# Performance work log

Hardware: AMD Instinct MI355X
Metric: run time of the kernel (lower is better)

Reference implementation:

```python
import jax, jax.numpy as jnp
import numpy as np

# DREAMPlace IDXST_IDCT (a.k.a. idsct2): y[u,v] = sum_p sum_q x[p,q] * sin(pi*p*(u+0.5)/M) * cos(pi*q*(v+0.5)/N)
# i.e. IDXST (inverse discrete sine transform, DST-III-like, unnormalized) along the M axis
# and IDCT (DCT-III-like, unnormalized, full weight on k=0) along the N axis.
# Computed with the classic 2N-padded FFT trick using the precomputed twiddles
# expk[k] = exp(-1j*pi*k/(2N)) stored as [N,2] (real, imag), matching precompute_expk.

def _idxt_spectrum(x, expk):
    """F[u] = sum_k x[k] * exp(-1j*pi*k*(2u+1)/(2N)), along last axis.
    Re(F) is the IDCT sum (cos), -Im(F) is the IDXST sum (sin)."""
    N = x.shape[-1]
    c = (x * expk[..., 0]) + 1j * (x * expk[..., 1])  # x[k] * exp(-j*pi*k/(2N))
    z = jnp.concatenate([c, jnp.zeros_like(c)], axis=-1)  # zero-pad to 2N
    return jnp.fft.fft(z, axis=-1)[..., :N]


def idct_1d(x, expk):
    # y[u] = sum_k x[k] cos(pi*k*(2u+1)/(2N))
    return _idxt_spectrum(x, expk).real


def idxst_1d(x, expk):
    # y[u] = sum_k x[k] sin(pi*k*(2u+1)/(2N))
    return -_idxt_spectrum(x, expk).imag


def _make_expk(L):
    k = jnp.arange(L, dtype=jnp.float32) * (np.pi / (2.0 * L))
    return jnp.stack([jnp.cos(k), -jnp.sin(k)], axis=-1)  # exp(-j*pi*k/(2L))


def setup_inputs() -> dict:
    M, N = 4096, 4096
    key = jax.random.key(0)
    x = jax.random.normal(key, (M, N), dtype=jnp.float32)
    return {"x": x, "expkM": _make_expk(M), "expkN": _make_expk(N)}


def reference(x, expkM, expkN):
    # IDCT along the last dim (N), then IDXST along the second-to-last dim (M):
    # idxst(idct(x)^T)^T
    t = idct_1d(x, expkN)                                        # [M, N]
    y = idxst_1d(t.swapaxes(-2, -1), expkM).swapaxes(-2, -1)     # [M, N]
    return y
```

## Files before the change

kernel.cpp:

```cpp
#include <hip/hip_runtime.h>
#include <hip/hip_bf16.h>
#include <stdint.h>
#include <cmath>


typedef __attribute__((ext_vector_type(4))) float f32x4;
typedef __attribute__((ext_vector_type(8))) unsigned short u16x8;
typedef __attribute__((ext_vector_type(8))) __bf16 bf16x8;

__device__ __forceinline__ unsigned short f2bf(float f) {
  union { float f; unsigned u; } v; v.f = f;
  unsigned u = v.u + 0x7fffu + ((v.u >> 16) & 1u);
  return (unsigned short)(u >> 16);
}

__device__ __forceinline__ void gen_half(int idx, u16x8* Pe, u16x8* Po,
                                         int isSin, int jshift, int jmask,
                                         unsigned mask4L, float sc) {
  int i = idx >> jshift;
  int jb = (idx & jmask) * 8;
  unsigned tp = 2u * (unsigned)i + 1u;
  unsigned re = (2u * (unsigned)jb * tp) & mask4L;
  unsigned ro = (re + tp) & mask4L;
  unsigned step = (2u * tp) & mask4L;
  u16x8 pe, po;
#pragma unroll
  for (int t = 0; t < 8; t++) {
    float se_, ce_, so_, co_;
    __sincosf((float)re * sc, &se_, &ce_);
    __sincosf((float)ro * sc, &so_, &co_);
    pe[t] = f2bf(isSin ? se_ : ce_);
    po[t] = f2bf(isSin ? so_ : co_);
    re = (re + step) & mask4L;
    ro = (ro + step) & mask4L;
  }
  Pe[idx] = pe;
  Po[idx] = po;
}

__global__ void prep_kernel(const f32x4* __restrict__ x, u16x8* __restrict__ xe,
                            u16x8* __restrict__ xo, u16x8* __restrict__ Ce,
                            u16x8* __restrict__ Co, u16x8* __restrict__ Se,
                            u16x8* __restrict__ So, int nConvBlocks,
                            int nGenNBlocks, int jshiftN, int jmaskN,
                            unsigned mask4N, float scN, int jshiftM, int jmaskM,
                            unsigned mask4M, float scM) {
  int b = blockIdx.x;
  if (b < nConvBlocks) {
    int idx = b * 256 + threadIdx.x;
    f32x4 a = x[4 * idx], bb = x[4 * idx + 1], c = x[4 * idx + 2],
          d = x[4 * idx + 3];
    u16x8 e, o;
    e[0] = f2bf(a[0]);  o[0] = f2bf(a[1]);  e[1] = f2bf(a[2]);  o[1] = f2bf(a[3]);
    e[2] = f2bf(bb[0]); o[2] = f2bf(bb[1]); e[3] = f2bf(bb[2]); o[3] = f2bf(bb[3]);
    e[4] = f2bf(c[0]);  o[4] = f2bf(c[1]);  e[5] = f2bf(c[2]);  o[5] = f2bf(c[3]);
    e[6] = f2bf(d[0]);  o[6] = f2bf(d[1]);  e[7] = f2bf(d[2]);  o[7] = f2bf(d[3]);
    xe[idx] = e;
    xo[idx] = o;
  } else if (b < nConvBlocks + nGenNBlocks) {
    int idx = (b - nConvBlocks) * 256 + threadIdx.x;
    gen_half(idx, Ce, Co, 0, jshiftN, jmaskN, mask4N, scN);
  } else {
    int idx = (b - nConvBlocks - nGenNBlocks) * 256 + threadIdx.x;
    gen_half(idx, Se, So, 1, jshiftM, jmaskM, mask4M, scM);
  }
}

#define LGKM8()                                             \
  do {                                                      \
    asm volatile("s_waitcnt lgkmcnt(8)" ::: "memory");      \
    __builtin_amdgcn_sched_barrier(0);                      \
  } while (0)
#define LGKM0()                                             \
  do {                                                      \
    asm volatile("s_waitcnt lgkmcnt(0)" ::: "memory");      \
    __builtin_amdgcn_sched_barrier(0);                      \
  } while (0)
#define VMCNT8()                                            \
  do {                                                      \
    asm volatile("s_waitcnt vmcnt(8)" ::: "memory");        \
    __builtin_amdgcn_sched_barrier(0);                      \
  } while (0)
#define VMCNT0()                                            \
  do {                                                      \
    asm volatile("s_waitcnt vmcnt(0)" ::: "memory");        \
    __builtin_amdgcn_sched_barrier(0);                      \
  } while (0)
#define BAR() __builtin_amdgcn_s_barrier()

template <int STAGE>
__global__ __launch_bounds__(256, 2) void fused_gemm_kernel(
    const unsigned short* __restrict__ Ae,
    const unsigned short* __restrict__ Ao,
    const unsigned short* __restrict__ Be,
    const unsigned short* __restrict__ Bo,
    unsigned short* __restrict__ out0, unsigned short* __restrict__ out1,
    int outStride, int K, int Lfull) {
  __shared__ unsigned short AsE[128 * 64];
  __shared__ unsigned short BsE[128 * 64];
  __shared__ unsigned short AsO[128 * 64];
  __shared__ unsigned short BsO[128 * 64];

  const int tid = threadIdx.x;

  const int nwg = gridDim.x * gridDim.y;
  const int lin = blockIdx.y * gridDim.x + blockIdx.x;
  int swb = lin;
  if ((nwg & 7) == 0) swb = (lin & 7) * (nwg >> 3) + (lin >> 3);
  const int m0 = (swb / gridDim.x) * 128;
  const int n0 = (swb % gridDim.x) * 128;

  const int wave = tid >> 6;
  const int lane = tid & 63;
  const int wm = (wave & 1) * 64;
  const int wn = (wave >> 1) * 64;
  const int l16 = lane & 15;
  const int quad = lane >> 4;
  const int swz = (quad ^ (l16 & 7)) * 8;

  const int lrow = lane >> 3;
  const int lsw = ((lane & 7) ^ lrow) * 8;

  auto stageP = [&](const unsigned short* __restrict__ A,
                    const unsigned short* __restrict__ B, unsigned short* As,
                    unsigned short* Bs, int k0) {
#define GLL(src, dst)                                                        \
  __builtin_amdgcn_global_load_lds(                                          \
      (const __attribute__((address_space(1))) void*)(src),                  \
      (__attribute__((address_space(3))) void*)(dst), 16, 0, 0)
#pragma unroll
    for (int t = 0; t < 4; t++) {
      int ch = wave + 4 * t;
      GLL(A + (size_t)(m0 + 8 * ch + lrow) * K + lsw + k0, As + ch * 512);
      GLL(B + (size_t)(n0 + 8 * ch + lrow) * K + lsw + k0, Bs + ch * 512);
    }
#undef GLL
  };

  f32x4 accE[4][4], accO[4][4];
#pragma unroll
  for (int i = 0; i < 4; i++)
#pragma unroll
    for (int j = 0; j < 4; j++) {
      accE[i][j] = f32x4{0.f, 0.f, 0.f, 0.f};
      accO[i][j] = f32x4{0.f, 0.f, 0.f, 0.f};
    }

  auto parity = [&](const unsigned short* As, const unsigned short* Bs,
                    f32x4 (&acc)[4][4]) {
    const int so0 = swz;
    const int so1 = swz ^ 32;
    bf16x8 a0[4], b0[4], a1[4], b1[4];
#pragma unroll
    for (int i = 0; i < 4; i++)
      a0[i] = *(const bf16x8*)(As + (wm + i * 16 + l16) * 64 + so0);
#pragma unroll
    for (int j = 0; j < 4; j++)
      b0[j] = *(const bf16x8*)(Bs + (wn + j * 16 + l16) * 64 + so0);
#pragma unroll
    for (int i = 0; i < 4; i++)
      a1[i] = *(const bf16x8*)(As + (wm + i * 16 + l16) * 64 + so1);
#pragma unroll
    for (int j = 0; j < 4; j++)
      b1[j] = *(const bf16x8*)(Bs + (wn + j * 16 + l16) * 64 + so1);
    LGKM8();
    __builtin_amdgcn_s_setprio(1);
#pragma unroll
    for (int i = 0; i < 4; i++)
#pragma unroll
      for (int j = 0; j < 4; j++)
        acc[i][j] = __builtin_amdgcn_mfma_f32_16x16x32_bf16(
            a0[i], b0[j], acc[i][j], 0, 0, 0);
    __builtin_amdgcn_s_setprio(0);
    LGKM0();
    __builtin_amdgcn_s_setprio(1);
#pragma unroll
    for (int i = 0; i < 4; i++)
#pragma unroll
      for (int j = 0; j < 4; j++)
        acc[i][j] = __builtin_amdgcn_mfma_f32_16x16x32_bf16(
            a1[i], b1[j], acc[i][j], 0, 0, 0);
    __builtin_amdgcn_s_setprio(0);
  };

  stageP(Ae, Be, AsE, BsE, 0);

  for (int k0 = 0; k0 < K; k0 += 64) {
    const bool lastIt = (k0 + 64 >= K);

    stageP(Ao, Bo, AsO, BsO, k0);
    VMCNT8();
    BAR();
    parity(AsE, BsE, accE);
    BAR();

    if (!lastIt) {
      stageP(Ae, Be, AsE, BsE, k0 + 64);
      VMCNT8();
    } else {
      VMCNT0();
    }
    BAR();
    parity(AsO, BsO, accO);
    BAR();
  }

#pragma unroll
  for (int i = 0; i < 4; i++) {
#pragma unroll
    for (int j = 0; j < 4; j++) {
      int n = n0 + wn + j * 16 + l16;
      int mb = m0 + wm + i * 16 + quad * 4;
#pragma unroll
      for (int r = 0; r < 4; r++) {
        float e = accE[i][j][r];
        float o = accO[i][j][r];
        int m = mb + r;
        if (STAGE == 1) {
          unsigned short* mat = (n & 1) ? out1 : out0;
          int c = n >> 1;
          mat[(size_t)m * outStride + c] = f2bf(e + o);
          mat[(size_t)(Lfull - 1 - m) * outStride + c] = f2bf(e - o);
        } else {
          float* y = (float*)out0;
          y[(size_t)m * outStride + n] = e + o;
          y[(size_t)(Lfull - 1 - m) * outStride + n] = o - e;
        }
      }
    }
  }
}

extern "C" void kernel_launch(void* const* d_in, const int* in_sizes, int n_in,
                              void* d_out, int out_size, void* d_ws,
                              size_t ws_size, hipStream_t stream) {
  const float* x = (const float*)d_in[0];
  const int M = in_sizes[1] / 2;
  const int N = in_sizes[2] / 2;
  const size_t MN = (size_t)M * N;

  unsigned short* ws = (unsigned short*)d_ws;
  unsigned short* xe = ws;
  unsigned short* xo = ws + MN / 2;
  unsigned short* Ce = ws + MN;
  unsigned short* Co = ws + MN + MN / 4;
  unsigned short* Se = ws + MN * 3 / 2;
  unsigned short* So = ws + MN * 7 / 4;
  unsigned short* tTe = ws + MN * 2;
  unsigned short* tTo = ws + MN * 5 / 2;

  int shiftN = 0; while ((1 << shiftN) < N) shiftN++;
  int shiftM = 0; while ((1 << shiftM) < M) shiftM++;

  int nConvBlocks = (int)(MN / 16 / 256);
  int nGenNBlocks = (N / 2) * (N / 2) / 8 / 256;
  int nGenMBlocks = (M / 2) * (M / 2) / 8 / 256;
  prep_kernel<<<nConvBlocks + nGenNBlocks + nGenMBlocks, 256, 0, stream>>>(
      (const f32x4*)x, (u16x8*)xe, (u16x8*)xo, (u16x8*)Ce, (u16x8*)Co,
      (u16x8*)Se, (u16x8*)So, nConvBlocks, nGenNBlocks, shiftN - 4,
      (N / 16) - 1, (unsigned)(4 * N - 1),
      (float)(3.14159265358979323846 / (2.0 * N)), shiftM - 4, (M / 16) - 1,
      (unsigned)(4 * M - 1), (float)(3.14159265358979323846 / (2.0 * M)));

  fused_gemm_kernel<1><<<dim3(M / 128, (N / 2) / 128), 256, 0, stream>>>(
      Ce, Co, xe, xo, tTe, tTo, M / 2, N / 2, N);

  fused_gemm_kernel<2><<<dim3(N / 128, (M / 2) / 128), 256, 0, stream>>>(
      Se, So, tTe, tTo, (unsigned short*)d_out, nullptr, N, M / 2, M);
}
```

Before: 266.6 us.

## Split GEMM block across eight waves and remap tiles per XCD

Each 128x128 GEMM workgroup now runs 8 waves (512 threads) instead of 4. Each wave computes a 64x32 sub-tile instead of 64x64. The load and LDS wait counts are reduced to match the fewer loads per thread. Separately, the block index is remapped so that each XCD gets a contiguous 8x8 patch of tiles for L2 locality. The goal is more resident waves to hide memory and LDS latency, at the cost of more LDS fragment reloads per MFMA and more barrier participants.

```diff
diff --git a/kernel.cpp b/kernel.cpp
--- a/kernel.cpp
+++ b/kernel.cpp
@@ -66,9 +66,9 @@
   }
 }
 
-#define LGKM8()                                             \
-  do {                                                      \
-    asm volatile("s_waitcnt lgkmcnt(8)" ::: "memory");      \
+#define LGKM6()                                             \
+  do {                                                      \
+    asm volatile("s_waitcnt lgkmcnt(6)" ::: "memory");      \
     __builtin_amdgcn_sched_barrier(0);                      \
   } while (0)
 #define LGKM0()                                             \
@@ -76,9 +76,9 @@
     asm volatile("s_waitcnt lgkmcnt(0)" ::: "memory");      \
     __builtin_amdgcn_sched_barrier(0);                      \
   } while (0)
-#define VMCNT8()                                            \
-  do {                                                      \
-    asm volatile("s_waitcnt vmcnt(8)" ::: "memory");        \
+#define VMCNT4()                                            \
+  do {                                                      \
+    asm volatile("s_waitcnt vmcnt(4)" ::: "memory");        \
     __builtin_amdgcn_sched_barrier(0);                      \
   } while (0)
 #define VMCNT0()                                            \
@@ -89,7 +89,7 @@
 #define BAR() __builtin_amdgcn_s_barrier()
 
 template <int STAGE>
-__global__ __launch_bounds__(256, 2) void fused_gemm_kernel(
+__global__ __launch_bounds__(512, 2) void fused_gemm_kernel(
     const unsigned short* __restrict__ Ae,
     const unsigned short* __restrict__ Ao,
     const unsigned short* __restrict__ Be,
@@ -103,17 +103,32 @@
 
   const int tid = threadIdx.x;
 
-  const int nwg = gridDim.x * gridDim.y;
-  const int lin = blockIdx.y * gridDim.x + blockIdx.x;
-  int swb = lin;
-  if ((nwg & 7) == 0) swb = (lin & 7) * (nwg >> 3) + (lin >> 3);
-  const int m0 = (swb / gridDim.x) * 128;
-  const int n0 = (swb % gridDim.x) * 128;
+  int bx = blockIdx.x, by = blockIdx.y;
+  {
+    const int gx = gridDim.x, gy = gridDim.y;
+    const int lin = by * gx + bx;
+    if ((gx % 8) == 0 && (gy % 8) == 0 && ((gx >> 3) * (gy >> 3)) == 8) {
+      const int xcd = lin & 7, idx = lin >> 3;
+      const int spx = gx >> 3;
+      const int sx = xcd % spx, sy = xcd / spx;
+      bx = sx * 8 + (idx & 7);
+      by = sy * 8 + (idx >> 3);
+    } else {
+      const int nwg = gx * gy;
+      if ((nwg & 7) == 0) {
+        const int swb = (lin & 7) * (nwg >> 3) + (lin >> 3);
+        bx = swb % gx;
+        by = swb / gx;
+      }
+    }
+  }
+  const int m0 = by * 128;
+  const int n0 = bx * 128;
 
   const int wave = tid >> 6;
   const int lane = tid & 63;
   const int wm = (wave & 1) * 64;
-  const int wn = (wave >> 1) * 64;
+  const int wn = (wave >> 1) * 32;
   const int l16 = lane & 15;
   const int quad = lane >> 4;
   const int swz = (quad ^ (l16 & 7)) * 8;
@@ -129,46 +144,46 @@
       (const __attribute__((address_space(1))) void*)(src),                  \
       (__attribute__((address_space(3))) void*)(dst), 16, 0, 0)
 #pragma unroll
-    for (int t = 0; t < 4; t++) {
-      int ch = wave + 4 * t;
+    for (int t = 0; t < 2; t++) {
+      int ch = wave + 8 * t;
       GLL(A + (size_t)(m0 + 8 * ch + lrow) * K + lsw + k0, As + ch * 512);
       GLL(B + (size_t)(n0 + 8 * ch + lrow) * K + lsw + k0, Bs + ch * 512);
     }
 #undef GLL
   };
 
-  f32x4 accE[4][4], accO[4][4];
+  f32x4 accE[4][2], accO[4][2];
 #pragma unroll
   for (int i = 0; i < 4; i++)
 #pragma unroll
-    for (int j = 0; j < 4; j++) {
+    for (int j = 0; j < 2; j++) {
       accE[i][j] = f32x4{0.f, 0.f, 0.f, 0.f};
       accO[i][j] = f32x4{0.f, 0.f, 0.f, 0.f};
     }
 
   auto parity = [&](const unsigned short* As, const unsigned short* Bs,
-                    f32x4 (&acc)[4][4]) {
+                    f32x4 (&acc)[4][2]) {
     const int so0 = swz;
     const int so1 = swz ^ 32;
-    bf16x8 a0[4], b0[4], a1[4], b1[4];
+    bf16x8 a0[4], b0[2], a1[4], b1[2];
 #pragma unroll
     for (int i = 0; i < 4; i++)
       a0[i] = *(const bf16x8*)(As + (wm + i * 16 + l16) * 64 + so0);
 #pragma unroll
-    for (int j = 0; j < 4; j++)
+    for (int j = 0; j < 2; j++)
       b0[j] = *(const bf16x8*)(Bs + (wn + j * 16 + l16) * 64 + so0);
 #pragma unroll
     for (int i = 0; i < 4; i++)
       a1[i] = *(const bf16x8*)(As + (wm + i * 16 + l16) * 64 + so1);
 #pragma unroll
-    for (int j = 0; j < 4; j++)
+    for (int j = 0; j < 2; j++)
       b1[j] = *(const bf16x8*)(Bs + (wn + j * 16 + l16) * 64 + so1);
-    LGKM8();
+    LGKM6();
     __builtin_amdgcn_s_setprio(1);
 #pragma unroll
     for (int i = 0; i < 4; i++)
 #pragma unroll
-      for (int j = 0; j < 4; j++)
+      for (int j = 0; j < 2; j++)
         acc[i][j] = __builtin_amdgcn_mfma_f32_16x16x32_bf16(
             a0[i], b0[j], acc[i][j], 0, 0, 0);
     __builtin_amdgcn_s_setprio(0);
@@ -177,7 +192,7 @@
 #pragma unroll
     for (int i = 0; i < 4; i++)
 #pragma unroll
-      for (int j = 0; j < 4; j++)
+      for (int j = 0; j < 2; j++)
         acc[i][j] = __builtin_amdgcn_mfma_f32_16x16x32_bf16(
             a1[i], b1[j], acc[i][j], 0, 0, 0);
     __builtin_amdgcn_s_setprio(0);
@@ -189,14 +204,14 @@
     const bool lastIt = (k0 + 64 >= K);
 
     stageP(Ao, Bo, AsO, BsO, k0);
-    VMCNT8();
+    VMCNT4();
     BAR();
     parity(AsE, BsE, accE);
     BAR();
 
     if (!lastIt) {
       stageP(Ae, Be, AsE, BsE, k0 + 64);
-      VMCNT8();
+      VMCNT4();
     } else {
       VMCNT0();
     }
@@ -208,7 +223,7 @@
 #pragma unroll
   for (int i = 0; i < 4; i++) {
 #pragma unroll
-    for (int j = 0; j < 4; j++) {
+    for (int j = 0; j < 2; j++) {
       int n = n0 + wn + j * 16 + l16;
       int mb = m0 + wm + i * 16 + quad * 4;
 #pragma unroll
@@ -262,9 +277,9 @@
       (float)(3.14159265358979323846 / (2.0 * N)), shiftM - 4, (M / 16) - 1,
       (unsigned)(4 * M - 1), (float)(3.14159265358979323846 / (2.0 * M)));
 
-  fused_gemm_kernel<1><<<dim3(M / 128, (N / 2) / 128), 256, 0, stream>>>(
+  fused_gemm_kernel<1><<<dim3(M / 128, (N / 2) / 128), 512, 0, stream>>>(
       Ce, Co, xe, xo, tTe, tTo, M / 2, N / 2, N);
 
-  fused_gemm_kernel<2><<<dim3(N / 128, (M / 2) / 128), 256, 0, stream>>>(
+  fused_gemm_kernel<2><<<dim3(N / 128, (M / 2) / 128), 512, 0, stream>>>(
       Se, So, tTe, tTo, (unsigned short*)d_out, nullptr, N, M / 2, M);
 }
```

New measurement: 317.6 us. +19.1%, slower.
